# Performance work log

Measured on AMD Instinct MI355X. Metric: run time of the kernel, lower is better.

The kernel has to match this reference:

```python
import jax, jax.numpy as jnp
import numpy as np

B, N, C, F, E, K = 2, 2048, 1024, 4096, 8, 2

def setup_inputs() -> dict:
    key = jax.random.key(0)
    k = jax.random.split(key, 6)
    xavier1 = float(np.sqrt(6.0 / (C + F)))
    xavier2 = float(np.sqrt(6.0 / (F + C)))
    return {
        "x": jax.random.normal(k[0], (B, N, C), dtype=jnp.float32),
        "router_w": jax.random.normal(k[1], (E, C), dtype=jnp.float32) * 0.01,
        "w1": jax.random.uniform(k[2], (E, F, C), dtype=jnp.float32, minval=-xavier1, maxval=xavier1),
        "b1": jnp.zeros((E, F), dtype=jnp.float32),
        "w2": jax.random.uniform(k[3], (E, C, F), dtype=jnp.float32, minval=-xavier2, maxval=xavier2),
        "b2": jnp.zeros((E, C), dtype=jnp.float32),
    }

def reference(x, router_w, w1, b1, w2, b2):
    Bb, Nn, Cc = x.shape
    x_flat = x.reshape(-1, Cc)                                   # [T, C]
    # Router (eval mode: no noise)
    logits = jnp.einsum('tc,ec->te', x_flat, router_w)           # [T, E]
    probs = jax.nn.softmax(logits, axis=-1)
    top_w, top_idx = jax.lax.top_k(probs, K)                     # [T, K]
    top_w = top_w / (jnp.sum(top_w, axis=-1, keepdims=True) + 1e-9)
    # Dense all-expert MLP (same math as the per-expert gather/scatter loop)
    h = jnp.einsum('tc,efc->tef', x_flat, w1) + b1[None]          # [T, E, F]
    h = jax.nn.relu(h)
    y = jnp.einsum('tef,ecf->tec', h, w2) + b2[None]              # [T, E, C]
    # Gather the K selected experts per token and combine
    sel = jnp.take_along_axis(y, top_idx[:, :, None], axis=1)    # [T, K, C]
    out = jnp.einsum('tkc,tk->tc', sel, top_w)                   # [T, C]
    return out.reshape(Bb, Nn, Cc)
```

## Files before the change

### kernel.cpp

```cpp
#include <hip/hip_runtime.h>
#include <hip/hip_fp16.h>


#define T_TOK 4096
#define C_DIM 1024
#define F_DIM 4096
#define E_NUM 8
#define MAXT 80
#define NP   (MAXT * 128)
#define TILE_H 8192

typedef float f32x4 __attribute__((ext_vector_type(4)));
typedef _Float16 half8 __attribute__((ext_vector_type(8)));
typedef _Float16 half4 __attribute__((ext_vector_type(4)));

#define AS1 __attribute__((address_space(1)))
#define AS3 __attribute__((address_space(3)))

__device__ __forceinline__ int swz(int r, int ec) { return ec ^ ((r & 7) << 3); }

__device__ __forceinline__ half8 cvt8(float4 f0, float4 f1) {
  half8 hv;
  hv[0] = (_Float16)f0.x; hv[1] = (_Float16)f0.y; hv[2] = (_Float16)f0.z; hv[3] = (_Float16)f0.w;
  hv[4] = (_Float16)f1.x; hv[5] = (_Float16)f1.y; hv[6] = (_Float16)f1.z; hv[7] = (_Float16)f1.w;
  return hv;
}

__device__ __forceinline__ int xcd_swz(int bid, int nwg) {
  int xcd = bid & 7, rest = bid >> 3;
  int q = nwg >> 3, r = nwg & 7;
  return (xcd < r ? xcd * (q + 1) : r * (q + 1) + (xcd - r) * q) + rest;
}

__global__ __launch_bounds__(256) void router_kernel(
    const float* __restrict__ x, const float* __restrict__ rw,
    int* __restrict__ top_idx, float* __restrict__ top_w)
{
  int t = blockIdx.x * 4 + (threadIdx.x >> 6);
  int lane = threadIdx.x & 63;
  const float* xr = x + (size_t)t * C_DIM;
  float acc[E_NUM];
#pragma unroll
  for (int e = 0; e < E_NUM; ++e) acc[e] = 0.f;
  for (int j = 0; j < C_DIM / 64; ++j) {
    int c = j * 64 + lane;
    float xv = xr[c];
#pragma unroll
    for (int e = 0; e < E_NUM; ++e) acc[e] += xv * rw[e * C_DIM + c];
  }
#pragma unroll
  for (int e = 0; e < E_NUM; ++e) {
    float v = acc[e];
#pragma unroll
    for (int off = 32; off > 0; off >>= 1) v += __shfl_xor(v, off);
    acc[e] = v;
  }
  if (lane == 0) {
    float mx = acc[0];
    for (int e = 1; e < E_NUM; ++e) mx = fmaxf(mx, acc[e]);
    float p[E_NUM]; float Z = 0.f;
    for (int e = 0; e < E_NUM; ++e) { p[e] = expf(acc[e] - mx); Z += p[e]; }
    int b0 = 0;
    for (int e = 1; e < E_NUM; ++e) if (p[e] > p[b0]) b0 = e;
    int b1i = -1; float pb = -1.f;
    for (int e = 0; e < E_NUM; ++e) if (e != b0 && p[e] > pb) { pb = p[e]; b1i = e; }
    float p0 = p[b0] / Z, p1 = pb / Z;
    float s = p0 + p1 + 1e-9f;
    top_idx[t * 2 + 0] = b0;
    top_idx[t * 2 + 1] = b1i;
    top_w[t * 2 + 0] = p0 / s;
    top_w[t * 2 + 1] = p1 / s;
  }
}

__global__ void build_lists(const int* __restrict__ top_idx,
                            int* __restrict__ rows_g, int* __restrict__ counts,
                            int* __restrict__ tile_off, int* __restrict__ inv)
{
  int e = threadIdx.x >> 6;
  int lane = threadIdx.x & 63;
  int cnt = 0;
  for (int t0 = 0; t0 < T_TOK; t0 += 64) {
    int t = t0 + lane;
    bool sel = (top_idx[t * 2] == e) || (top_idx[t * 2 + 1] == e);
    cnt += __popcll(__ballot(sel));
  }
  if (lane == 0) counts[e] = cnt;
  __syncthreads();
  if (threadIdx.x == 0) {
    int o = 0;
    for (int i = 0; i < E_NUM; ++i) { tile_off[i] = o; o += 2 * ((counts[i] + 255) >> 8); }
    tile_off[E_NUM] = o;
  }
  __syncthreads();
  int base = tile_off[e] * 128;
  int pos = 0;
  for (int t0 = 0; t0 < T_TOK; t0 += 64) {
    int t = t0 + lane;
    int i0 = top_idx[t * 2], i1 = top_idx[t * 2 + 1];
    bool sel = (i0 == e) || (i1 == e);
    unsigned long long mask = __ballot(sel);
    if (sel) {
      int p = pos + __popcll(mask & ((1ull << lane) - 1ull));
      int slot = t * 2 + ((i0 == e) ? 0 : 1);
      rows_g[base + p] = slot;
      inv[slot] = (e << 16) | (base + p);
    }
    pos += __popcll(mask);
  }
}

__global__ __launch_bounds__(256) void gather_x(
    const float* __restrict__ x, const int* __restrict__ rows_g,
    const int* __restrict__ counts, const int* __restrict__ tile_off,
    _Float16* __restrict__ xg)
{
  unsigned g = blockIdx.x * 256 + threadIdx.x;
  unsigned p = g >> 7, ccr = g & 127;
  int gt = p >> 7, r = p & 127;
  int kc = ccr >> 3, c8 = ccr & 7;
  int e = -1;
#pragma unroll
  for (int i = 0; i < E_NUM; ++i)
    if (gt >= tile_off[i] && gt < tile_off[i + 1]) e = i;
  half8 hv = {};
  if (e >= 0) {
    int nrem = counts[e] - (gt - tile_off[e]) * 128;
    if (r < nrem) {
      int t = rows_g[p] >> 1;
      const float4* s = reinterpret_cast<const float4*>(x + (size_t)t * C_DIM + kc * 64 + c8 * 8);
      hv = cvt8(s[0], s[1]);
    }
  }
  *reinterpret_cast<half8*>(xg + ((size_t)gt * 16 + kc) * TILE_H + r * 64 + ((c8 ^ (r & 7)) << 3)) = hv;
}

__global__ __launch_bounds__(256) void cvt_w(
    const float* __restrict__ w1, const float* __restrict__ w2,
    _Float16* __restrict__ w1t, _Float16* __restrict__ w2t,
    int ch, int Fc, int lgnftl, int lgnkc, unsigned halfChunks)
{
  unsigned g = blockIdx.x * 256 + threadIdx.x;
  if (g < halfChunks) {
    unsigned tile = g >> 10;
    unsigned kc = tile & 15;
    unsigned et = tile >> 4;
    unsigned ftl = et & ((1u << lgnftl) - 1);
    unsigned e = et >> lgnftl;
    unsigned r = (g >> 3) & 127;
    unsigned sc = g & 7;
    unsigned c8 = sc ^ (r & 7);
    unsigned frow = ftl * 128 + r;
    const float4* s = reinterpret_cast<const float4*>(
        w1 + ((size_t)e * F_DIM + ch * Fc + frow) * C_DIM + kc * 64 + c8 * 8);
    *reinterpret_cast<half8*>(w1t + (size_t)g * 8) = cvt8(s[0], s[1]);
  } else {
    unsigned g2 = g - halfChunks;
    unsigned tile = g2 >> 10;
    unsigned kc = tile & ((1u << lgnkc) - 1);
    unsigned et = tile >> lgnkc;
    unsigned ct = et & 7;
    unsigned e = et >> 3;
    unsigned r = (g2 >> 3) & 127;
    unsigned sc = g2 & 7;
    unsigned c8 = sc ^ (r & 7);
    unsigned c = ct * 128 + r;
    const float4* s = reinterpret_cast<const float4*>(
        w2 + ((size_t)e * C_DIM + c) * F_DIM + ch * Fc + kc * 64 + c8 * 8);
    *reinterpret_cast<half8*>(w2t + (size_t)g2 * 8) = cvt8(s[0], s[1]);
  }
}

#define STAGE4(a0_, a1_, b0_, b1_)                                                \
  {                                                                               \
    _Pragma("unroll")                                                             \
    for (int i_ = 0; i_ < 2; ++i_) {                                              \
      int o_ = tid * 8 + i_ * 4096;                                               \
      __builtin_amdgcn_global_load_lds((const AS1 void*)((a0_) + o_),             \
          (AS3 void*)(&As[o_]), 16, 0, 0);                                        \
      __builtin_amdgcn_global_load_lds((const AS1 void*)((a1_) + o_),             \
          (AS3 void*)(&As[8192 + o_]), 16, 0, 0);                                 \
      __builtin_amdgcn_global_load_lds((const AS1 void*)((b0_) + o_),             \
          (AS3 void*)(&Bs[o_]), 16, 0, 0);                                        \
      __builtin_amdgcn_global_load_lds((const AS1 void*)((b1_) + o_),             \
          (AS3 void*)(&Bs[8192 + o_]), 16, 0, 0);                                 \
    }                                                                             \
  }

#define COMPUTE256()                                                              \
  _Pragma("unroll")                                                               \
  for (int kk = 0; kk < 64; kk += 32) {                                           \
    const int klo = kk + (lane >> 4) * 8;                                         \
    half8 aF[8], bF[4];                                                           \
    _Pragma("unroll")                                                             \
    for (int m = 0; m < 8; ++m) {                                                 \
      int r = m * 16 + (lane & 15);                                               \
      aF[m] = *reinterpret_cast<const half8*>(&As[wr * 8192 + r * 64 + swz(r, klo)]); \
    }                                                                             \
    _Pragma("unroll")                                                             \
    for (int n = 0; n < 4; ++n) {                                                 \
      int rb = (wc & 1) * 64 + n * 16 + (lane & 15);                              \
      bF[n] = *reinterpret_cast<const half8*>(&Bs[(wc >> 1) * 8192 + rb * 64 + swz(rb, klo)]); \
    }                                                                             \
    _Pragma("unroll")                                                             \
    for (int m = 0; m < 8; ++m)                                                   \
      _Pragma("unroll")                                                           \
      for (int n = 0; n < 4; ++n)                                                 \
        acc[m][n] = __builtin_amdgcn_mfma_f32_16x16x32_f16(bF[n], aF[m], acc[m][n], 0, 0, 0); \
  }

__global__ __launch_bounds__(512, 2) void gemm1_kernel(
    const _Float16* __restrict__ xg, const _Float16* __restrict__ w1t,
    const float* __restrict__ b1, const int* __restrict__ tile_off,
    _Float16* __restrict__ ht, int ch, int Fc)
{
  const int NFT = Fc >> 8;
  const int wgid = xcd_swz(blockIdx.x, gridDim.x);
  const int grp = wgid / (4 * NFT);
  const int rem = wgid - grp * 4 * NFT;
  const int ft = rem >> 2;
  const int gt = (grp * 4 + (rem & 3)) * 2;
  if (gt >= tile_off[E_NUM]) return;
  int e = 0;
  while (gt >= tile_off[e + 1]) ++e;
  const int nftl = Fc >> 7;
  const _Float16* At0 = xg + (size_t)gt * 16 * TILE_H;
  const _Float16* At1 = xg + (size_t)(gt + 1) * 16 * TILE_H;
  const _Float16* Bt0 = w1t + (size_t)(e * nftl + 2 * ft) * 16 * TILE_H;
  const _Float16* Bt1 = w1t + (size_t)(e * nftl + 2 * ft + 1) * 16 * TILE_H;

  __shared__ __align__(16) _Float16 As[2 * TILE_H];
  __shared__ __align__(16) _Float16 Bs[2 * TILE_H];

  const int tid = threadIdx.x;
  const int lane = tid & 63;
  const int wave = tid >> 6;
  const int wr = wave >> 2, wc = wave & 3;

  f32x4 acc[8][4];
#pragma unroll
  for (int m = 0; m < 8; ++m)
#pragma unroll
    for (int n = 0; n < 4; ++n) acc[m][n] = (f32x4){0.f, 0.f, 0.f, 0.f};

  for (int kc = 0; kc < 16; ++kc) {
    size_t ko = (size_t)kc * TILE_H;
    STAGE4(At0 + ko, At1 + ko, Bt0 + ko, Bt1 + ko);
    __syncthreads();
    COMPUTE256();
    __syncthreads();
  }

  const int nkcF = Fc >> 6;
  const int gtw = gt + wr;
  const float* b1e = b1 + e * F_DIM + ch * Fc;
#pragma unroll
  for (int m = 0; m < 8; ++m) {
    int tok = m * 16 + (lane & 15);
#pragma unroll
    for (int n = 0; n < 4; ++n) {
      int flb = ft * 256 + wc * 64 + n * 16 + ((lane >> 4) << 2);
      float4 bv = *reinterpret_cast<const float4*>(b1e + flb);
      half4 hv;
      hv[0] = (_Float16)fmaxf(acc[m][n][0] + bv.x, 0.f);
      hv[1] = (_Float16)fmaxf(acc[m][n][1] + bv.y, 0.f);
      hv[2] = (_Float16)fmaxf(acc[m][n][2] + bv.z, 0.f);
      hv[3] = (_Float16)fmaxf(acc[m][n][3] + bv.w, 0.f);
      *reinterpret_cast<half4*>(
          ht + ((size_t)gtw * nkcF + (flb >> 6)) * TILE_H + tok * 64 +
          ((((flb >> 3) & 7) ^ (tok & 7)) << 3) + (flb & 7)) = hv;
    }
  }
}

__global__ __launch_bounds__(512, 2) void gemm2_kernel(
    const _Float16* __restrict__ ht, const _Float16* __restrict__ w2t,
    const int* __restrict__ tile_off, _Float16* __restrict__ y,
    int Fc, int kspl, int accum)
{
  const int wgid = xcd_swz(blockIdx.x, gridDim.x);
  const int NCMB = 4 * kspl;
  const int grp = wgid / (4 * NCMB);
  const int rem = wgid - grp * 4 * NCMB;
  const int cmb = rem >> 2;
  const int gt = (grp * 4 + (rem & 3)) * 2;
  if (gt >= tile_off[E_NUM]) return;
  const int ct2 = cmb & 3;
  const int ks = cmb >> 2;
  int e = 0;
  while (gt >= tile_off[e + 1]) ++e;
  const int nkc = Fc >> 6;
  const int klen = nkc / kspl;
  const _Float16* At0 = ht + ((size_t)gt * nkc + ks * klen) * TILE_H;
  const _Float16* At1 = ht + ((size_t)(gt + 1) * nkc + ks * klen) * TILE_H;
  const _Float16* Bt0 = w2t + ((size_t)(e * 8 + 2 * ct2) * nkc + ks * klen) * TILE_H;
  const _Float16* Bt1 = w2t + ((size_t)(e * 8 + 2 * ct2 + 1) * nkc + ks * klen) * TILE_H;

  __shared__ __align__(16) _Float16 As[2 * TILE_H];
  __shared__ __align__(16) _Float16 Bs[2 * TILE_H];

  const int tid = threadIdx.x;
  const int lane = tid & 63;
  const int wave = tid >> 6;
  const int wr = wave >> 2, wc = wave & 3;

  f32x4 acc[8][4];
#pragma unroll
  for (int m = 0; m < 8; ++m)
#pragma unroll
    for (int n = 0; n < 4; ++n) acc[m][n] = (f32x4){0.f, 0.f, 0.f, 0.f};

  for (int kc = 0; kc < klen; ++kc) {
    size_t ko = (size_t)kc * TILE_H;
    STAGE4(At0 + ko, At1 + ko, Bt0 + ko, Bt1 + ko);
    __syncthreads();
    COMPUTE256();
    __syncthreads();
  }

  _Float16* yk = y + ((size_t)(ks * MAXT + gt + wr) * 128) * C_DIM;
#pragma unroll
  for (int m = 0; m < 8; ++m) {
    int tok = m * 16 + (lane & 15);
#pragma unroll
    for (int n = 0; n < 4; ++n) {
      int cb = ct2 * 256 + wc * 64 + n * 16 + ((lane >> 4) << 2);
      half4* p = reinterpret_cast<half4*>(yk + (size_t)tok * C_DIM + cb);
      half4 hv;
      if (accum) {
        half4 old = *p;
        hv[0] = (_Float16)(acc[m][n][0] + (float)old[0]);
        hv[1] = (_Float16)(acc[m][n][1] + (float)old[1]);
        hv[2] = (_Float16)(acc[m][n][2] + (float)old[2]);
        hv[3] = (_Float16)(acc[m][n][3] + (float)old[3]);
      } else {
        hv[0] = (_Float16)acc[m][n][0];
        hv[1] = (_Float16)acc[m][n][1];
        hv[2] = (_Float16)acc[m][n][2];
        hv[3] = (_Float16)acc[m][n][3];
      }
      *p = hv;
    }
  }
}

__global__ __launch_bounds__(256) void combine_kernel(
    const _Float16* __restrict__ y, const int* __restrict__ inv,
    const float* __restrict__ top_w, const float* __restrict__ b2,
    float* __restrict__ out, int kspl)
{
  int g = blockIdx.x * 256 + threadIdx.x;
  int t = g >> 7, c8 = (g & 127) << 3;
  float o[8];
#pragma unroll
  for (int i = 0; i < 8; ++i) o[i] = 0.f;
#pragma unroll
  for (int k = 0; k < 2; ++k) {
    int iv = inv[t * 2 + k];
    int e = iv >> 16, pos = iv & 0xffff;
    float w = top_w[t * 2 + k];
    const float4* bb = reinterpret_cast<const float4*>(b2 + e * C_DIM + c8);
    float4 bv0 = bb[0], bv1 = bb[1];
    float s[8] = {bv0.x, bv0.y, bv0.z, bv0.w, bv1.x, bv1.y, bv1.z, bv1.w};
    for (int ks = 0; ks < kspl; ++ks) {
      half8 hv = *reinterpret_cast<const half8*>(
          y + ((size_t)(ks * MAXT * 128 + pos)) * C_DIM + c8);
#pragma unroll
      for (int i = 0; i < 8; ++i) s[i] += (float)hv[i];
    }
#pragma unroll
    for (int i = 0; i < 8; ++i) o[i] += w * s[i];
  }
  float4* op = reinterpret_cast<float4*>(out + (size_t)t * C_DIM + c8);
  op[0] = (float4){o[0], o[1], o[2], o[3]};
  op[1] = (float4){o[4], o[5], o[6], o[7]};
}

extern "C" void kernel_launch(void* const* d_in, const int* in_sizes, int n_in,
                              void* d_out, int out_size, void* d_ws, size_t ws_size,
                              hipStream_t stream)
{
  const float* x  = (const float*)d_in[0];
  const float* rw = (const float*)d_in[1];
  const float* w1 = (const float*)d_in[2];
  const float* b1 = (const float*)d_in[3];
  const float* w2 = (const float*)d_in[4];
  const float* b2 = (const float*)d_in[5];
  float* out = (float*)d_out;

  char* ws = (char*)d_ws;
  size_t off = 0;
  auto carve = [&](size_t bytes) -> void* {
    void* p = ws + off;
    off += (bytes + 255) & ~(size_t)255;
    return p;
  };
  int*   top_idx  = (int*)carve((size_t)T_TOK * 2 * sizeof(int));
  float* top_w    = (float*)carve((size_t)T_TOK * 2 * sizeof(float));
  int*   counts   = (int*)carve(E_NUM * sizeof(int));
  int*   tile_off = (int*)carve((E_NUM + 1) * sizeof(int));
  int*   rows_g   = (int*)carve((size_t)NP * sizeof(int));
  int*   inv      = (int*)carve((size_t)T_TOK * 2 * sizeof(int));
  _Float16* xg    = (_Float16*)carve((size_t)MAXT * 16 * TILE_H * sizeof(_Float16));
  _Float16* y     = (_Float16*)carve((size_t)2 * NP * C_DIM * sizeof(_Float16));
  size_t fixed = off;

  int nchunk = 8;
  const int cands[4] = {1, 2, 4, 8};
  for (int ci = 0; ci < 4; ++ci) {
    int n = cands[ci];
    size_t fc = (size_t)(F_DIM / n);
    size_t w1b = ((size_t)E_NUM * fc * C_DIM * 2 + 255) & ~(size_t)255;
    size_t w2b = ((size_t)E_NUM * C_DIM * fc * 2 + 255) & ~(size_t)255;
    size_t htb = ((size_t)MAXT * (fc >> 6) * TILE_H * 2 + 255) & ~(size_t)255;
    if (fixed + w1b + w2b + htb <= ws_size) { nchunk = n; break; }
  }
  const int Fc = F_DIM / nchunk;
  int lgFc = 0; while ((1 << lgFc) < Fc) ++lgFc;
  _Float16* w1t = (_Float16*)carve((size_t)E_NUM * Fc * C_DIM * sizeof(_Float16));
  _Float16* w2t = (_Float16*)carve((size_t)E_NUM * C_DIM * Fc * sizeof(_Float16));
  _Float16* ht  = (_Float16*)carve((size_t)MAXT * (Fc >> 6) * TILE_H * sizeof(_Float16));

  const int kspl = (Fc >= 2048) ? 2 : 1;

  router_kernel<<<T_TOK / 4, 256, 0, stream>>>(x, rw, top_idx, top_w);
  build_lists<<<1, 512, 0, stream>>>(top_idx, rows_g, counts, tile_off, inv);
  gather_x<<<(MAXT * 128 * 128) / 256, 256, 0, stream>>>(x, rows_g, counts, tile_off, xg);

  const unsigned halfChunks = (unsigned)Fc << 10;
  for (int ch = 0; ch < nchunk; ++ch) {
    cvt_w<<<8 * Fc, 256, 0, stream>>>(w1, w2, w1t, w2t, ch, Fc, lgFc - 7, lgFc - 6, halfChunks);
    gemm1_kernel<<<(MAXT / 2) * (Fc / 256), 512, 0, stream>>>(
        xg, w1t, b1, tile_off, ht, ch, Fc);
    gemm2_kernel<<<(MAXT / 2) * 4 * kspl, 512, 0, stream>>>(
        ht, w2t, tile_off, y, Fc, kspl, ch != 0);
  }
  combine_kernel<<<(T_TOK * 128) / 256, 256, 0, stream>>>(y, inv, top_w, b2, out, kspl);
}
```

Baseline: 431.6 us.

## Double-buffer LDS tiles in both GEMMs and double the gemm2 K-split

Moves the A/B staging tiles into dynamic LDS with two buffers, so the next K-chunk's global-to-LDS loads are issued before computing on the current chunk, and drops one barrier per iteration. This is meant to hide global load latency behind the MFMA work. It also raises the gemm2 K-split (1→2 or 2→4) and doubles the y workspace so gemm2 launches more workgroups, at the cost of more partial-sum traffic in combine. LDS per block grows to 128 KB, which likely halves occupancy from the two blocks per CU the launch bounds ask for.

```diff
diff --git a/kernel.cpp b/kernel.cpp
--- a/kernel.cpp
+++ b/kernel.cpp
@@ -171,36 +171,40 @@
   }
 }
 
-#define STAGE4(a0_, a1_, b0_, b1_)                                                \
+#define LDS_T(buf_, ix_) (lds + ((size_t)((buf_) * 4 + (ix_))) * TILE_H)
+
+#define STAGE4(buf_, a0_, a1_, b0_, b1_)                                          \
   {                                                                               \
     _Pragma("unroll")                                                             \
     for (int i_ = 0; i_ < 2; ++i_) {                                              \
       int o_ = tid * 8 + i_ * 4096;                                               \
       __builtin_amdgcn_global_load_lds((const AS1 void*)((a0_) + o_),             \
-          (AS3 void*)(&As[o_]), 16, 0, 0);                                        \
+          (AS3 void*)(LDS_T(buf_, 0) + o_), 16, 0, 0);                            \
       __builtin_amdgcn_global_load_lds((const AS1 void*)((a1_) + o_),             \
-          (AS3 void*)(&As[8192 + o_]), 16, 0, 0);                                 \
+          (AS3 void*)(LDS_T(buf_, 1) + o_), 16, 0, 0);                            \
       __builtin_amdgcn_global_load_lds((const AS1 void*)((b0_) + o_),             \
-          (AS3 void*)(&Bs[o_]), 16, 0, 0);                                        \
+          (AS3 void*)(LDS_T(buf_, 2) + o_), 16, 0, 0);                            \
       __builtin_amdgcn_global_load_lds((const AS1 void*)((b1_) + o_),             \
-          (AS3 void*)(&Bs[8192 + o_]), 16, 0, 0);                                 \
+          (AS3 void*)(LDS_T(buf_, 3) + o_), 16, 0, 0);                            \
     }                                                                             \
   }
 
-#define COMPUTE256()                                                              \
+#define COMPUTE256(buf_)                                                          \
   _Pragma("unroll")                                                               \
   for (int kk = 0; kk < 64; kk += 32) {                                           \
     const int klo = kk + (lane >> 4) * 8;                                         \
     half8 aF[8], bF[4];                                                           \
+    const _Float16* aT_ = LDS_T(buf_, wr);                                        \
+    const _Float16* bT_ = LDS_T(buf_, 2 + (wc >> 1));                             \
     _Pragma("unroll")                                                             \
     for (int m = 0; m < 8; ++m) {                                                 \
       int r = m * 16 + (lane & 15);                                               \
-      aF[m] = *reinterpret_cast<const half8*>(&As[wr * 8192 + r * 64 + swz(r, klo)]); \
+      aF[m] = *reinterpret_cast<const half8*>(&aT_[r * 64 + swz(r, klo)]);        \
     }                                                                             \
     _Pragma("unroll")                                                             \
     for (int n = 0; n < 4; ++n) {                                                 \
       int rb = (wc & 1) * 64 + n * 16 + (lane & 15);                              \
-      bF[n] = *reinterpret_cast<const half8*>(&Bs[(wc >> 1) * 8192 + rb * 64 + swz(rb, klo)]); \
+      bF[n] = *reinterpret_cast<const half8*>(&bT_[rb * 64 + swz(rb, klo)]);      \
     }                                                                             \
     _Pragma("unroll")                                                             \
     for (int m = 0; m < 8; ++m)                                                   \
@@ -214,6 +218,7 @@
     const float* __restrict__ b1, const int* __restrict__ tile_off,
     _Float16* __restrict__ ht, int ch, int Fc)
 {
+  extern __shared__ _Float16 lds[];
   const int NFT = Fc >> 8;
   const int wgid = xcd_swz(blockIdx.x, gridDim.x);
   const int grp = wgid / (4 * NFT);
@@ -229,9 +234,6 @@
   const _Float16* Bt0 = w1t + (size_t)(e * nftl + 2 * ft) * 16 * TILE_H;
   const _Float16* Bt1 = w1t + (size_t)(e * nftl + 2 * ft + 1) * 16 * TILE_H;
 
-  __shared__ __align__(16) _Float16 As[2 * TILE_H];
-  __shared__ __align__(16) _Float16 Bs[2 * TILE_H];
-
   const int tid = threadIdx.x;
   const int lane = tid & 63;
   const int wave = tid >> 6;
@@ -243,11 +245,15 @@
 #pragma unroll
     for (int n = 0; n < 4; ++n) acc[m][n] = (f32x4){0.f, 0.f, 0.f, 0.f};
 
+  STAGE4(0, At0, At1, Bt0, Bt1);
+  __syncthreads();
   for (int kc = 0; kc < 16; ++kc) {
-    size_t ko = (size_t)kc * TILE_H;
-    STAGE4(At0 + ko, At1 + ko, Bt0 + ko, Bt1 + ko);
-    __syncthreads();
-    COMPUTE256();
+    const int cur = kc & 1;
+    if (kc + 1 < 16) {
+      size_t ko = (size_t)(kc + 1) * TILE_H;
+      STAGE4(cur ^ 1, At0 + ko, At1 + ko, Bt0 + ko, Bt1 + ko);
+    }
+    COMPUTE256(cur);
     __syncthreads();
   }
 
@@ -278,6 +284,7 @@
     const int* __restrict__ tile_off, _Float16* __restrict__ y,
     int Fc, int kspl, int accum)
 {
+  extern __shared__ _Float16 lds[];
   const int wgid = xcd_swz(blockIdx.x, gridDim.x);
   const int NCMB = 4 * kspl;
   const int grp = wgid / (4 * NCMB);
@@ -296,9 +303,6 @@
   const _Float16* Bt0 = w2t + ((size_t)(e * 8 + 2 * ct2) * nkc + ks * klen) * TILE_H;
   const _Float16* Bt1 = w2t + ((size_t)(e * 8 + 2 * ct2 + 1) * nkc + ks * klen) * TILE_H;
 
-  __shared__ __align__(16) _Float16 As[2 * TILE_H];
-  __shared__ __align__(16) _Float16 Bs[2 * TILE_H];
-
   const int tid = threadIdx.x;
   const int lane = tid & 63;
   const int wave = tid >> 6;
@@ -310,11 +314,15 @@
 #pragma unroll
     for (int n = 0; n < 4; ++n) acc[m][n] = (f32x4){0.f, 0.f, 0.f, 0.f};
 
+  STAGE4(0, At0, At1, Bt0, Bt1);
+  __syncthreads();
   for (int kc = 0; kc < klen; ++kc) {
-    size_t ko = (size_t)kc * TILE_H;
-    STAGE4(At0 + ko, At1 + ko, Bt0 + ko, Bt1 + ko);
-    __syncthreads();
-    COMPUTE256();
+    const int cur = kc & 1;
+    if (kc + 1 < klen) {
+      size_t ko = (size_t)(kc + 1) * TILE_H;
+      STAGE4(cur ^ 1, At0 + ko, At1 + ko, Bt0 + ko, Bt1 + ko);
+    }
+    COMPUTE256(cur);
     __syncthreads();
   }
 
@@ -402,7 +410,7 @@
   int*   rows_g   = (int*)carve((size_t)NP * sizeof(int));
   int*   inv      = (int*)carve((size_t)T_TOK * 2 * sizeof(int));
   _Float16* xg    = (_Float16*)carve((size_t)MAXT * 16 * TILE_H * sizeof(_Float16));
-  _Float16* y     = (_Float16*)carve((size_t)2 * NP * C_DIM * sizeof(_Float16));
+  _Float16* y     = (_Float16*)carve((size_t)4 * NP * C_DIM * sizeof(_Float16));
   size_t fixed = off;
 
   int nchunk = 8;
@@ -421,7 +429,8 @@
   _Float16* w2t = (_Float16*)carve((size_t)E_NUM * C_DIM * Fc * sizeof(_Float16));
   _Float16* ht  = (_Float16*)carve((size_t)MAXT * (Fc >> 6) * TILE_H * sizeof(_Float16));
 
-  const int kspl = (Fc >= 2048) ? 2 : 1;
+  const int kspl = (Fc >= 2048) ? 4 : 2;
+  const size_t dynLds = (size_t)8 * TILE_H * sizeof(_Float16);
 
   router_kernel<<<T_TOK / 4, 256, 0, stream>>>(x, rw, top_idx, top_w);
   build_lists<<<1, 512, 0, stream>>>(top_idx, rows_g, counts, tile_off, inv);
@@ -430,9 +439,9 @@
   const unsigned halfChunks = (unsigned)Fc << 10;
   for (int ch = 0; ch < nchunk; ++ch) {
     cvt_w<<<8 * Fc, 256, 0, stream>>>(w1, w2, w1t, w2t, ch, Fc, lgFc - 7, lgFc - 6, halfChunks);
-    gemm1_kernel<<<(MAXT / 2) * (Fc / 256), 512, 0, stream>>>(
+    gemm1_kernel<<<(MAXT / 2) * (Fc / 256), 512, dynLds, stream>>>(
         xg, w1t, b1, tile_off, ht, ch, Fc);
-    gemm2_kernel<<<(MAXT / 2) * 4 * kspl, 512, 0, stream>>>(
+    gemm2_kernel<<<(MAXT / 2) * 4 * kspl, 512, dynLds, stream>>>(
         ht, w2t, tile_off, y, Fc, kspl, ch != 0);
   }
   combine_kernel<<<(T_TOK * 128) / 256, 256, 0, stream>>>(y, inv, top_w, b2, out, kspl);
```

New measurement: 354.4 us. -17.9%, faster.
